# Kernel optimization log

Measured on AMD Instinct MI355X. Metric: run time of the kernel, lower is better.

## Reference

```python
import jax, jax.numpy as jnp
import numpy as np

B, S, L = 8, 64, 6          # graphs, spatial side, orientation layers
K = 6                       # Chebyshev order
IN_D, HID, OUT_D = 3, 128, 10


def _grid_edges(num_graphs, s, l):
    b, o, y, x = np.meshgrid(np.arange(num_graphs), np.arange(l), np.arange(s), np.arange(s), indexing='ij')
    nid = ((b * l + o) * s + y) * s + x  # linear node id, [B,L,s,s]
    srcs, dsts = [], []
    def add(a, c):
        srcs.append(a.ravel()); dsts.append(c.ravel())
    add(nid[..., :-1], nid[..., 1:]); add(nid[..., 1:], nid[..., :-1])                 # x-neighbors
    add(nid[:, :, :-1, :], nid[:, :, 1:, :]); add(nid[:, :, 1:, :], nid[:, :, :-1, :])  # y-neighbors
    nxt = np.roll(nid, -1, axis=1)                                                     # orientation ring
    add(nid, nxt); add(nxt, nid)
    return np.stack([np.concatenate(srcs), np.concatenate(dsts)]).astype(np.int32)


def _cluster_spatial(num_graphs, s, l):
    b, o, y, x = np.meshgrid(np.arange(num_graphs), np.arange(l), np.arange(s), np.arange(s), indexing='ij')
    h = s // 2
    return (((b * l + o) * h + y // 2) * h + x // 2).ravel().astype(np.int32)


def setup_inputs() -> dict:
    key = jax.random.key(0)
    ks = jax.random.split(key, 20)
    inp = {}
    N1 = B * L * S * S
    inp['x'] = jax.random.normal(ks[0], (N1, IN_D), jnp.float32)
    for i, s in enumerate([S, S // 2, S // 4]):
        ei = _grid_edges(B, s, L)
        inp[f'edge_index{i+1}'] = jnp.asarray(ei)
        inp[f'edge_attr{i+1}'] = jax.random.uniform(ks[1 + i], (ei.shape[1],), jnp.float32, 0.1, 1.0)
    inp['cluster1'] = jnp.asarray(_cluster_spatial(B, S, L))
    inp['cluster2'] = jnp.asarray(_cluster_spatial(B, S // 2, L))
    inp['cluster3'] = jnp.asarray(_cluster_spatial(B, S // 4, L))
    s4 = S // 8
    b, o, y, x = np.meshgrid(np.arange(B), np.arange(L), np.arange(s4), np.arange(s4), indexing='ij')
    inp['cluster4'] = jnp.asarray(((b * s4 + y) * s4 + x).ravel().astype(np.int32))  # collapse orientation axis
    inp['batch_final'] = jnp.asarray(np.repeat(np.arange(B), s4 * s4).astype(np.int32))
    dims = [(IN_D, HID), (HID, HID), (HID, HID), (HID, HID), (HID, HID), (HID, OUT_D)]
    for i, (di, do) in enumerate(dims):
        inp[f'W{i+1}'] = jax.random.normal(ks[8 + i], (K, di, do), jnp.float32) / np.float32(np.sqrt(di * K))
        inp[f'b{i+1}'] = jnp.zeros((do,), jnp.float32)
    for i in range(5):
        inp[f'gamma{i+1}'] = jnp.ones((HID,), jnp.float32)
        inp[f'beta{i+1}'] = jnp.zeros((HID,), jnp.float32)
    return inp


def _cheb_conv(x, ei, ea, W, b):
    # Chebyshev polynomial graph conv: out = sum_k T_k(L) x @ W_k + b,
    # with T0=x, T1=Lx, Tk = 2 L T_{k-1} - T_{k-2}; L applied via edge gather/scatter.
    src, dst = ei[0], ei[1]
    n = x.shape[0]
    def lap(v):
        return jax.ops.segment_sum(ea[:, None] * v[src], dst, num_segments=n)
    Tx0 = x
    out = Tx0 @ W[0]
    Tx1 = lap(x)
    out = out + Tx1 @ W[1]
    for k in range(2, W.shape[0]):
        Tx2 = 2.0 * lap(Tx1) - Tx0
        out = out + Tx2 @ W[k]
        Tx0, Tx1 = Tx1, Tx2
    return out + b


def _bn(x, g, bt):
    # BatchNorm1d in training mode (batch statistics, biased variance, eps=1e-5)
    mu = x.mean(0)
    var = x.var(0)
    return g * (x - mu) * jax.lax.rsqrt(var + 1e-5) + bt


def reference(x, edge_index1, edge_attr1, edge_index2, edge_attr2, edge_index3, edge_attr3, cluster1, cluster2, cluster3, cluster4, batch_final, W1, b1, W2, b2, W3, b3, W4, b4, W5, b5, W6, b6, gamma1, beta1, gamma2, beta2, gamma3, beta3, gamma4, beta4, gamma5, beta5):
    h = jax.nn.relu(_bn(_cheb_conv(x, edge_index1, edge_attr1, W1, b1), gamma1, beta1))
    h = jax.nn.relu(_bn(_cheb_conv(h, edge_index1, edge_attr1, W2, b2), gamma2, beta2))
    h = jax.ops.segment_max(h, cluster1, num_segments=B * L * (S // 2) ** 2)
    h = jax.nn.relu(_bn(_cheb_conv(h, edge_index2, edge_attr2, W3, b3), gamma3, beta3))
    h = jax.nn.relu(_bn(_cheb_conv(h, edge_index2, edge_attr2, W4, b4), gamma4, beta4))
    h = jax.ops.segment_max(h, cluster2, num_segments=B * L * (S // 4) ** 2)
    h = jax.nn.relu(_bn(_cheb_conv(h, edge_index3, edge_attr3, W5, b5), gamma5, beta5))
    h = jax.nn.relu(_cheb_conv(h, edge_index3, edge_attr3, W6, b6))
    h = jax.ops.segment_max(h, cluster3, num_segments=B * L * (S // 8) ** 2)   # spatial pool 3
    h = jax.ops.segment_max(h, cluster4, num_segments=B * (S // 8) ** 2)        # orientation pool
    g = jax.ops.segment_max(h, batch_final, num_segments=B)                     # global max pool
    return jax.nn.log_softmax(g, axis=1)
```

## Files before the change

### kernel.cpp

```cpp
#include <hip/hip_runtime.h>
#include <math.h>

#define L_OR 6
#define N_BL 48

typedef unsigned short u16;
typedef __attribute__((ext_vector_type(8))) short s8v;
typedef __attribute__((ext_vector_type(4))) float f4v;

#define N1 196608
#define N2 49152
#define N3 12288
#define LSTRIDE 114688

__device__ u16   g_cat[(size_t)N1 * 768 + 1024];
__device__ u16   g_O[(size_t)N1 * 128];
__device__ float g_Tt[5 * (size_t)N1 * 3];
__device__ u16   g_Bt[4 * LSTRIDE];
__device__ u16   g_W6t[16 * 768];
__device__ float g_wt1[(size_t)N1 * 8];
__device__ float g_wt2[(size_t)N2 * 8];
__device__ float g_wt3[(size_t)N3 * 8];
__device__ float g_O10[(size_t)N3 * 10];
__device__ float g_part[1536 * 256];
__device__ float g_part2[64 * 256];
__device__ float g_gsc[128];
__device__ float g_gso[128];
__device__ unsigned g_cnt;

__device__ __forceinline__ float b2f(u16 v) {
    return __uint_as_float(((unsigned)v) << 16);
}
__device__ __forceinline__ u16 f2b(float f) {
    unsigned u = __float_as_uint(f);
    return (u16)((u + 0x7FFFu + ((u >> 16) & 1u)) >> 16);
}

__global__ __launch_bounds__(256)
void eaprep_all(float* __restrict__ wt1, float* __restrict__ wt2,
                float* __restrict__ wt3, const float* __restrict__ ea1,
                const float* __restrict__ ea2, const float* __restrict__ ea3)
{
    int idx = blockIdx.x * 256 + threadIdx.x;
    int S, n; float* wtab; const float* ea;
    if (idx < N1)            { S = 64; wtab = wt1; ea = ea1; n = idx; }
    else if (idx < N1 + N2)  { S = 32; wtab = wt2; ea = ea2; n = idx - N1; }
    else if (idx < N1 + N2 + N3) { S = 16; wtab = wt3; ea = ea3; n = idx - N1 - N2; }
    else return;
    int x = n % S, y = (n / S) % S, g = n / (S * S);
    int o = g % L_OR, b = g / L_OR;
    const int szx = N_BL * S * (S - 1);
    const int basex = (g * S + y) * (S - 1);
    float wxm = (x > 0)     ? ea[basex + x - 1] : 0.f;
    float wxp = (x < S - 1) ? ea[szx + basex + x] : 0.f;
    float wym = (y > 0)     ? ea[2 * szx + (g * (S - 1) + y - 1) * S + x] : 0.f;
    float wyp = (y < S - 1) ? ea[3 * szx + (g * (S - 1) + y) * S + x] : 0.f;
    int op_ = (o == 0) ? L_OR - 1 : o - 1;
    int on_ = (o == L_OR - 1) ? 0 : o + 1;
    int sp = ((b * L_OR + op_) * S + y) * S + x;
    int sn = ((b * L_OR + on_) * S + y) * S + x;
    float wom = ea[4 * szx + sp];
    float wop = ea[4 * szx + N_BL * S * S + n];
    float* w = wtab + (size_t)n * 8;
    w[0] = wxm; w[1] = wxp; w[2] = wym; w[3] = wyp; w[4] = wom; w[5] = wop;
    ((int*)w)[6] = sp - n;
    ((int*)w)[7] = sn - n;
}

template<int S>
__global__ __launch_bounds__(256)
void lap128b(u16* __restrict__ cat, int outSlot, int inSlot, int tppSlot,
             const float* __restrict__ wtab, float alpha)
{
    const int NN = N_BL * S * S;
    int node = blockIdx.x * 16 + (threadIdx.x >> 4);
    int c8   = threadIdx.x & 15;

    float4 wa = *(const float4*)(wtab + (size_t)node * 8);
    float4 wb = *(const float4*)(wtab + (size_t)node * 8 + 4);
    int dsp = __float_as_int(wb.z);
    int dsn = __float_as_int(wb.w);
    int sxm = (node > 0)      ? node - 1 : 0;
    int sxp = (node < NN - 1) ? node + 1 : node;
    int sym = (node >= S)     ? node - S : node;
    int syp = (node < NN - S) ? node + S : node;

    const int chOff = inSlot * 128 + c8 * 8;
    float a[8] = {0.f, 0.f, 0.f, 0.f, 0.f, 0.f, 0.f, 0.f};
    auto gather = [&](int src, float w) {
        s8v v = *(const s8v*)(cat + (size_t)src * 768 + chOff);
#pragma unroll
        for (int j = 0; j < 8; ++j) a[j] += w * b2f((u16)v[j]);
    };
    gather(sxm, wa.x); gather(sxp, wa.y); gather(sym, wa.z); gather(syp, wa.w);
    gather(node + dsp, wb.x); gather(node + dsn, wb.y);

    float r[8];
#pragma unroll
    for (int j = 0; j < 8; ++j) r[j] = alpha * a[j];
    if (tppSlot >= 0) {
        s8v t = *(const s8v*)(cat + (size_t)node * 768 + tppSlot * 128 + c8 * 8);
#pragma unroll
        for (int j = 0; j < 8; ++j) r[j] -= b2f((u16)t[j]);
    }
    uint4 ov;
    asm("v_cvt_pk_bf16_f32 %0, %1, %2" : "=v"(ov.x) : "v"(r[0]), "v"(r[1]));
    asm("v_cvt_pk_bf16_f32 %0, %1, %2" : "=v"(ov.y) : "v"(r[2]), "v"(r[3]));
    asm("v_cvt_pk_bf16_f32 %0, %1, %2" : "=v"(ov.z) : "v"(r[4]), "v"(r[5]));
    asm("v_cvt_pk_bf16_f32 %0, %1, %2" : "=v"(ov.w) : "v"(r[6]), "v"(r[7]));
    *(uint4*)(cat + (size_t)node * 768 + outSlot * 128 + c8 * 8) = ov;
}

template<int S>
__global__ __launch_bounds__(256)
void lap1bn(u16* __restrict__ cat, const u16* __restrict__ O,
            int t0Slot, int t1Slot, const float* __restrict__ wtab,
            const float* __restrict__ gsc, const float* __restrict__ gso)
{
    const int NN = N_BL * S * S;
    int node = blockIdx.x * 16 + (threadIdx.x >> 4);
    int c8   = threadIdx.x & 15;

    float4 wa = *(const float4*)(wtab + (size_t)node * 8);
    float4 wb = *(const float4*)(wtab + (size_t)node * 8 + 4);
    int dsp = __float_as_int(wb.z);
    int dsn = __float_as_int(wb.w);
    int sxm = (node > 0)      ? node - 1 : 0;
    int sxp = (node < NN - 1) ? node + 1 : node;
    int sym = (node >= S)     ? node - S : node;
    int syp = (node < NN - S) ? node + S : node;

    float sc[8], so[8];
    {
        float4 s0 = *(const float4*)(gsc + c8 * 8);
        float4 s1 = *(const float4*)(gsc + c8 * 8 + 4);
        float4 o0 = *(const float4*)(gso + c8 * 8);
        float4 o1 = *(const float4*)(gso + c8 * 8 + 4);
        sc[0]=s0.x; sc[1]=s0.y; sc[2]=s0.z; sc[3]=s0.w;
        sc[4]=s1.x; sc[5]=s1.y; sc[6]=s1.z; sc[7]=s1.w;
        so[0]=o0.x; so[1]=o0.y; so[2]=o0.z; so[3]=o0.w;
        so[4]=o1.x; so[5]=o1.y; so[6]=o1.z; so[7]=o1.w;
    }

    float a[8] = {0.f, 0.f, 0.f, 0.f, 0.f, 0.f, 0.f, 0.f};
    auto gatherbn = [&](int src, float w) {
        s8v v = *(const s8v*)(O + (size_t)src * 128 + c8 * 8);
#pragma unroll
        for (int j = 0; j < 8; ++j)
            a[j] += w * fmaxf(b2f((u16)v[j]) * sc[j] + so[j], 0.f);
    };
    gatherbn(sxm, wa.x); gatherbn(sxp, wa.y); gatherbn(sym, wa.z); gatherbn(syp, wa.w);
    gatherbn(node + dsp, wb.x); gatherbn(node + dsn, wb.y);

    float t0[8];
    {
        s8v v = *(const s8v*)(O + (size_t)node * 128 + c8 * 8);
#pragma unroll
        for (int j = 0; j < 8; ++j)
            t0[j] = fmaxf(b2f((u16)v[j]) * sc[j] + so[j], 0.f);
    }
    uint4 o0v, o1v;
    asm("v_cvt_pk_bf16_f32 %0, %1, %2" : "=v"(o0v.x) : "v"(t0[0]), "v"(t0[1]));
    asm("v_cvt_pk_bf16_f32 %0, %1, %2" : "=v"(o0v.y) : "v"(t0[2]), "v"(t0[3]));
    asm("v_cvt_pk_bf16_f32 %0, %1, %2" : "=v"(o0v.z) : "v"(t0[4]), "v"(t0[5]));
    asm("v_cvt_pk_bf16_f32 %0, %1, %2" : "=v"(o0v.w) : "v"(t0[6]), "v"(t0[7]));
    asm("v_cvt_pk_bf16_f32 %0, %1, %2" : "=v"(o1v.x) : "v"(a[0]), "v"(a[1]));
    asm("v_cvt_pk_bf16_f32 %0, %1, %2" : "=v"(o1v.y) : "v"(a[2]), "v"(a[3]));
    asm("v_cvt_pk_bf16_f32 %0, %1, %2" : "=v"(o1v.z) : "v"(a[4]), "v"(a[5]));
    asm("v_cvt_pk_bf16_f32 %0, %1, %2" : "=v"(o1v.w) : "v"(a[6]), "v"(a[7]));
    *(uint4*)(cat + (size_t)node * 768 + t0Slot * 128 + c8 * 8) = o0v;
    *(uint4*)(cat + (size_t)node * 768 + t1Slot * 128 + c8 * 8) = o1v;
}

template<int S>
__global__ __launch_bounds__(256)
void lap3_kernel(float* __restrict__ out, const float* __restrict__ in,
                 const float* __restrict__ tpp, const float* __restrict__ wtab,
                 float alpha)
{
    const int NN = N_BL * S * S;
    int n = blockIdx.x * 256 + threadIdx.x;
    if (n >= NN) return;
    float4 wa = *(const float4*)(wtab + (size_t)n * 8);
    float4 wb = *(const float4*)(wtab + (size_t)n * 8 + 4);
    int dsp = __float_as_int(wb.z);
    int dsn = __float_as_int(wb.w);
    int sxm = (n > 0)      ? n - 1 : 0;
    int sxp = (n < NN - 1) ? n + 1 : n;
    int sym = (n >= S)     ? n - S : n;
    int syp = (n < NN - S) ? n + S : n;

    float a0 = 0.f, a1 = 0.f, a2 = 0.f;
    auto gather = [&](int src, float w) {
        a0 += w * in[src * 3 + 0];
        a1 += w * in[src * 3 + 1];
        a2 += w * in[src * 3 + 2];
    };
    gather(sxm, wa.x); gather(sxp, wa.y); gather(sym, wa.z); gather(syp, wa.w);
    gather(n + dsp, wb.x); gather(n + dsn, wb.y);

    float r0 = alpha * a0, r1 = alpha * a1, r2 = alpha * a2;
    if (tpp) { r0 -= tpp[n * 3 + 0]; r1 -= tpp[n * 3 + 1]; r2 -= tpp[n * 3 + 2]; }
    out[n * 3 + 0] = r0; out[n * 3 + 1] = r1; out[n * 3 + 2] = r2;
}

__global__ __launch_bounds__(256)
void gemm_mfma_cat(u16* __restrict__ O, const u16* __restrict__ A,
                   const u16* __restrict__ Bf, const float* __restrict__ bias,
                   float* __restrict__ partials)
{
    __shared__ u16 Bs[2][8192];
    const int tid  = threadIdx.x;
    const int wave = tid >> 6;
    const int lane = tid & 63;
    const int lrow = lane & 15;
    const int kg   = lane >> 4;
    const int r0   = blockIdx.x * 128 + wave * 32;

    const u16* A0 = A + (size_t)(r0 + lrow) * 768 + kg * 8;
    const u16* A1 = A0 + (size_t)16 * 768;

    f4v acc[2][8] = {};

    auto stage = [&](int q, int slot) {
        const char* src = (const char*)(Bf + q * 8192) + wave * 4096 + lane * 16;
        char* dstb = (char*)(&Bs[slot][0]) + wave * 4096;
#pragma unroll
        for (int i = 0; i < 4; ++i)
            __builtin_amdgcn_global_load_lds(
                (const __attribute__((address_space(1))) unsigned*)(src + i * 1024),
                (__attribute__((address_space(3))) unsigned*)(dstb + i * 1024),
                16, 0, 0);
    };

    stage(0, 0);
    s8v a00 = *(const s8v*)(A0);
    s8v a10 = *(const s8v*)(A1);
    s8v a01 = *(const s8v*)(A0 + 32);
    s8v a11 = *(const s8v*)(A1 + 32);
    __syncthreads();

#pragma unroll 1
    for (int p = 0; p < 12; ++p) {
        stage(p + 1, (p + 1) & 1);
        s8v na00 = *(const s8v*)(A0 + (p + 1) * 64);
        s8v na10 = *(const s8v*)(A1 + (p + 1) * 64);
        s8v na01 = *(const s8v*)(A0 + (p + 1) * 64 + 32);
        s8v na11 = *(const s8v*)(A1 + (p + 1) * 64 + 32);
        const u16* bsl = &Bs[p & 1][0];
#pragma unroll
        for (int ct = 0; ct < 8; ++ct) {
            s8v b = *(const s8v*)&bsl[(ct * 64 + lane) * 8];
            acc[0][ct] = __builtin_amdgcn_mfma_f32_16x16x32_bf16(a00, b, acc[0][ct], 0, 0, 0);
            acc[1][ct] = __builtin_amdgcn_mfma_f32_16x16x32_bf16(a10, b, acc[1][ct], 0, 0, 0);
        }
#pragma unroll
        for (int ct = 0; ct < 8; ++ct) {
            s8v b = *(const s8v*)&bsl[4096 + (ct * 64 + lane) * 8];
            acc[0][ct] = __builtin_amdgcn_mfma_f32_16x16x32_bf16(a01, b, acc[0][ct], 0, 0, 0);
            acc[1][ct] = __builtin_amdgcn_mfma_f32_16x16x32_bf16(a11, b, acc[1][ct], 0, 0, 0);
        }
        __syncthreads();
        a00 = na00; a10 = na10; a01 = na01; a11 = na11;
    }

    __shared__ float sred[4][2][8][16];
    float cs[8], cq[8];
#pragma unroll
    for (int ct = 0; ct < 8; ++ct) { cs[ct] = 0.f; cq[ct] = 0.f; }

#pragma unroll
    for (int s = 0; s < 2; ++s)
#pragma unroll
        for (int ct = 0; ct < 8; ++ct) {
            int col = ct * 16 + lrow;
            float bv = bias[col];
#pragma unroll
            for (int j = 0; j < 4; ++j) {
                int row = r0 + s * 16 + kg * 4 + j;
                float v = acc[s][ct][j] + bv;
                O[(size_t)row * 128 + col] = f2b(v);
                cs[ct] += v; cq[ct] += v * v;
            }
        }
#pragma unroll
    for (int ct = 0; ct < 8; ++ct) {
        cs[ct] += __shfl_xor(cs[ct], 16); cs[ct] += __shfl_xor(cs[ct], 32);
        cq[ct] += __shfl_xor(cq[ct], 16); cq[ct] += __shfl_xor(cq[ct], 32);
    }
    if (lane < 16) {
#pragma unroll
        for (int ct = 0; ct < 8; ++ct) {
            sred[wave][0][ct][lane] = cs[ct];
            sred[wave][1][ct][lane] = cq[ct];
        }
    }
    __syncthreads();
    if (threadIdx.x < 128) {
        int ct = threadIdx.x >> 4, lr = threadIdx.x & 15;
        float S = 0.f, Q = 0.f;
#pragma unroll
        for (int w = 0; w < 4; ++w) { S += sred[w][0][ct][lr]; Q += sred[w][1][ct][lr]; }
        partials[blockIdx.x * 256 + threadIdx.x]       = S;
        partials[blockIdx.x * 256 + 128 + threadIdx.x] = Q;
    }
}

__global__ __launch_bounds__(256)
void wprep_all(const float* __restrict__ W2, const float* __restrict__ W3,
               const float* __restrict__ W4, const float* __restrict__ W5,
               const float* __restrict__ W6, u16* __restrict__ Bf,
               u16* __restrict__ W6t)
{
    int l = blockIdx.y;
    int idx = blockIdx.x * 256 + threadIdx.x;
    if (l == 4) {
        if (idx >= 16 * 768) return;
        int c = idx / 768, kk = idx % 768;
        int slot = kk >> 7, d = kk & 127;
        W6t[idx] = (c < 10) ? f2b(W6[(size_t)slot * 1280 + d * 10 + c]) : (u16)0;
        return;
    }
    const float* W = (l == 0) ? W2 : (l == 1) ? W3 : (l == 2) ? W4 : W5;
    int base = (l & 1) ? 5 : 0;
    int j    = idx & 7;
    int lane = (idx >> 3) & 63;
    int ct   = (idx >> 9) & 7;
    int k0s  = idx >> 12;
    int k    = k0s * 32 + (lane >> 4) * 8 + j;
    int col  = ct * 16 + (lane & 15);
    int slot = k >> 7, d = k & 127;
    int wk = slot - base; if (wk < 0) wk += 6;
    Bf[(size_t)l * LSTRIDE + idx] = f2b(W[(size_t)wk * 16384 + d * 128 + col]);
}

__global__ __launch_bounds__(256)
void l1gemm(u16* __restrict__ O, const float* __restrict__ T0,
            const float* __restrict__ Tt, const float* __restrict__ W,
            const float* __restrict__ bias, float* __restrict__ partials)
{
    __shared__ float Ts[128][18];
    __shared__ float sh[2][128], sh2[2][128];
    int tid = threadIdx.x;
    int rbase = blockIdx.x * 128;
    for (int i = tid; i < 128 * 18; i += 256) {
        int r = i / 18, t = i % 18;
        int k = t / 3, j = t % 3;
        Ts[r][t] = (k == 0) ? T0[(size_t)(rbase + r) * 3 + j]
                            : Tt[(size_t)(k - 1) * N1 * 3 + (size_t)(rbase + r) * 3 + j];
    }
    __syncthreads();
    int c = tid & 127, h = tid >> 7;
    float w[18];
#pragma unroll
    for (int k = 0; k < 6; ++k)
#pragma unroll
        for (int j = 0; j < 3; ++j) w[k * 3 + j] = W[(size_t)k * 384 + j * 128 + c];
    float bv = bias[c];
    float S = 0.f, Q = 0.f;
    for (int i = 0; i < 64; ++i) {
        int r = h * 64 + i;
        float acc = bv;
#pragma unroll
        for (int t = 0; t < 18; ++t) acc += Ts[r][t] * w[t];
        O[(size_t)(rbase + r) * 128 + c] = f2b(acc);
        S += acc; Q += acc * acc;
    }
    sh[h][c] = S; sh2[h][c] = Q;
    __syncthreads();
    if (tid < 128) {
        partials[blockIdx.x * 256 + tid]       = sh[0][tid] + sh[1][tid];
        partials[blockIdx.x * 256 + 128 + tid] = sh2[0][tid] + sh2[1][tid];
    }
}

__global__ __launch_bounds__(256)
void out10_cat(float* __restrict__ O10, const u16* __restrict__ cat,
               const u16* __restrict__ W6t, const float* __restrict__ bias)
{
    int col = threadIdx.x & 15;
    int row = blockIdx.x * 16 + (threadIdx.x >> 4);
    const u16* a = cat + (size_t)row * 768;
    const u16* w = W6t + (size_t)col * 768;
    float acc = 0.f;
#pragma unroll 4
    for (int k0 = 0; k0 < 768; k0 += 8) {
        s8v av = *(const s8v*)(a + k0);
        s8v wv = *(const s8v*)(w + k0);
#pragma unroll
        for (int j = 0; j < 8; ++j)
            acc += b2f((u16)av[j]) * b2f((u16)wv[j]);
    }
    if (col < 10)
        O10[(size_t)row * 10 + col] = fmaxf(acc + bias[col], 0.f);
}

__global__ __launch_bounds__(256)
void bn_reduce_f(const float* __restrict__ partials, int nblk, int N,
                 const float* __restrict__ g, const float* __restrict__ bt,
                 float* __restrict__ gsc, float* __restrict__ gso,
                 float* __restrict__ part2, unsigned* __restrict__ cnt)
{
    int tid = threadIdx.x;
    float S = 0.f;
#pragma unroll 4
    for (int b = blockIdx.x; b < nblk; b += 64)
        S += partials[(size_t)b * 256 + tid];
    part2[blockIdx.x * 256 + tid] = S;
    __threadfence();
    __syncthreads();
    __shared__ int last;
    if (tid == 0) last = (atomicAdd(cnt, 1u) == 63u) ? 1 : 0;
    __syncthreads();
    if (!last) return;
    __threadfence();
    int c = tid & 127, h = tid >> 7;
    float Sa = 0.f, Qa = 0.f;
#pragma unroll 8
    for (int b = h; b < 64; b += 2) {
        Sa += part2[b * 256 + c];
        Qa += part2[b * 256 + 128 + c];
    }
    __shared__ float shS[2][128], shQ[2][128];
    shS[h][c] = Sa; shQ[h][c] = Qa;
    __syncthreads();
    if (tid < 128) {
        float Sx = shS[0][tid] + shS[1][tid];
        float Qx = shQ[0][tid] + shQ[1][tid];
        float inv_n = 1.f / (float)N;
        float mu = Sx * inv_n;
        float var = Qx * inv_n - mu * mu;
        float is = rsqrtf(var + 1e-5f);
        float sc = is * g[tid];
        gsc[tid] = sc;
        gso[tid] = bt[tid] - mu * sc;
    }
    if (tid == 0) *cnt = 0u;
}

__global__ __launch_bounds__(256)
void bn_apply_pool8(const u16* __restrict__ O, u16* __restrict__ cat, int outSlot,
                    int s, int Nout,
                    const float* __restrict__ gsc, const float* __restrict__ gso)
{
    int idx = blockIdx.x * 256 + threadIdx.x;
    if (idx >= Nout * 16) return;
    int c8 = idx & 15;
    int n2 = idx >> 4;
    int h  = s >> 1;
    int x2 = n2 % h;
    int y2 = (n2 / h) % h;
    int gg = n2 / (h * h);
    int base = (gg * s + 2 * y2) * s + 2 * x2;
    s8v v0 = *(const s8v*)(O + (size_t)base * 128 + c8 * 8);
    s8v v1 = *(const s8v*)(O + (size_t)(base + 1) * 128 + c8 * 8);
    s8v v2 = *(const s8v*)(O + (size_t)(base + s) * 128 + c8 * 8);
    s8v v3 = *(const s8v*)(O + (size_t)(base + s + 1) * 128 + c8 * 8);
    s8v ov;
#pragma unroll
    for (int j = 0; j < 8; ++j) {
        int c = c8 * 8 + j;
        float sc = gsc[c], so = gso[c];
        float m =          b2f((u16)v0[j]) * sc + so;
        m = fmaxf(m, b2f((u16)v1[j]) * sc + so);
        m = fmaxf(m, b2f((u16)v2[j]) * sc + so);
        m = fmaxf(m, b2f((u16)v3[j]) * sc + so);
        ov[j] = (short)f2b(fmaxf(m, 0.f));
    }
    *(s8v*)(cat + (size_t)n2 * 768 + outSlot * 128 + c8 * 8) = ov;
}

__global__ __launch_bounds__(512)
void tail_fused(const float* __restrict__ O10, float* __restrict__ out)
{
    __shared__ float p4[512][10];
    __shared__ float G[8][10];
    __shared__ float rowm[8], rowl[8];
    int t = threadIdx.x;
    for (int i = t; i < 5120; i += 512) {
        int c = i % 10, n = i / 10;
        int x = n & 7, y = (n >> 3) & 7, b = n >> 6;
        float m = -INFINITY;
        for (int o = 0; o < L_OR; ++o) {
            int base = ((b * L_OR + o) * 16 + 2 * y) * 16 + 2 * x;
            m = fmaxf(m, O10[(size_t)base * 10 + c]);
            m = fmaxf(m, O10[(size_t)(base + 1) * 10 + c]);
            m = fmaxf(m, O10[(size_t)(base + 16) * 10 + c]);
            m = fmaxf(m, O10[(size_t)(base + 17) * 10 + c]);
        }
        p4[n][c] = m;
    }
    __syncthreads();
    if (t < 80) {
        int b = t / 10, c = t % 10;
        float m = -INFINITY;
        for (int p = 0; p < 64; ++p) m = fmaxf(m, p4[b * 64 + p][c]);
        G[b][c] = m;
    }
    __syncthreads();
    if (t < 8) {
        float m = -INFINITY;
        for (int c = 0; c < 10; ++c) m = fmaxf(m, G[t][c]);
        float s = 0.f;
        for (int c = 0; c < 10; ++c) s += expf(G[t][c] - m);
        rowm[t] = m; rowl[t] = logf(s);
    }
    __syncthreads();
    if (t < 80) {
        int b = t / 10, c = t % 10;
        out[t] = G[b][c] - rowm[b] - rowl[b];
    }
}

static void launch_lapb(u16* cat, int os, int is, int ts, const float* wtab,
                        int S, int N, float alpha, hipStream_t st)
{
    dim3 grid(N / 16), block(256);
    if (S == 64)      hipLaunchKernelGGL(lap128b<64>, grid, block, 0, st, cat, os, is, ts, wtab, alpha);
    else if (S == 32) hipLaunchKernelGGL(lap128b<32>, grid, block, 0, st, cat, os, is, ts, wtab, alpha);
    else              hipLaunchKernelGGL(lap128b<16>, grid, block, 0, st, cat, os, is, ts, wtab, alpha);
}

static void cheb_laps_b5(u16* cat, const float* wtab, int S, int N, hipStream_t st)
{
    for (int k = 1; k < 6; ++k) {
        int os = (k + 5) % 6;
        int is = (k - 1 + 5) % 6;
        int ts = (k >= 2) ? (k - 2 + 5) % 6 : -1;
        launch_lapb(cat, os, is, ts, wtab, S, N, (k == 1) ? 1.f : 2.f, st);
    }
}

static void cheb_laps_2to5(u16* cat, const float* wtab, int S, int N, hipStream_t st)
{
    for (int k = 2; k < 6; ++k)
        launch_lapb(cat, k, k - 1, k - 2, wtab, S, N, 2.f, st);
}

static void launch_lap1bn(u16* cat, const u16* O, const float* wtab,
                          const float* gsc, const float* gso,
                          int S, int N, hipStream_t st)
{
    dim3 grid(N / 16), block(256);
    if (S == 64)      hipLaunchKernelGGL(lap1bn<64>, grid, block, 0, st, cat, O, 0, 1, wtab, gsc, gso);
    else if (S == 32) hipLaunchKernelGGL(lap1bn<32>, grid, block, 0, st, cat, O, 0, 1, wtab, gsc, gso);
    else              hipLaunchKernelGGL(lap1bn<16>, grid, block, 0, st, cat, O, 0, 1, wtab, gsc, gso);
}

extern "C" void kernel_launch(void* const* d_in, const int* in_sizes, int n_in,
                              void* d_out, int out_size, void* d_ws, size_t ws_size,
                              hipStream_t stream)
{
    const float* x   = (const float*)d_in[0];
    const float* ea1 = (const float*)d_in[2];
    const float* ea2 = (const float*)d_in[4];
    const float* ea3 = (const float*)d_in[6];
    const float* W1  = (const float*)d_in[12];
    const float* b1  = (const float*)d_in[13];
    const float* W2  = (const float*)d_in[14];
    const float* b2  = (const float*)d_in[15];
    const float* W3  = (const float*)d_in[16];
    const float* b3  = (const float*)d_in[17];
    const float* W4  = (const float*)d_in[18];
    const float* b4  = (const float*)d_in[19];
    const float* W5  = (const float*)d_in[20];
    const float* b5  = (const float*)d_in[21];
    const float* W6  = (const float*)d_in[22];
    const float* b6  = (const float*)d_in[23];
    const float* g1  = (const float*)d_in[24];
    const float* be1 = (const float*)d_in[25];
    const float* g2  = (const float*)d_in[26];
    const float* be2 = (const float*)d_in[27];
    const float* g3  = (const float*)d_in[28];
    const float* be3 = (const float*)d_in[29];
    const float* g4  = (const float*)d_in[30];
    const float* be4 = (const float*)d_in[31];
    const float* g5  = (const float*)d_in[32];
    const float* be5 = (const float*)d_in[33];

    u16 *cat, *O, *Bt, *W6t;
    float *Tt, *O10, *part, *part2, *gsc, *gso, *wt1, *wt2, *wt3;
    unsigned* cnt;
    if (hipGetSymbolAddress((void**)&cat, HIP_SYMBOL(g_cat)) != hipSuccess) return;
    if (hipGetSymbolAddress((void**)&O,   HIP_SYMBOL(g_O))   != hipSuccess) return;
    if (hipGetSymbolAddress((void**)&Tt,  HIP_SYMBOL(g_Tt))  != hipSuccess) return;
    if (hipGetSymbolAddress((void**)&Bt,  HIP_SYMBOL(g_Bt))  != hipSuccess) return;
    if (hipGetSymbolAddress((void**)&W6t, HIP_SYMBOL(g_W6t)) != hipSuccess) return;
    if (hipGetSymbolAddress((void**)&O10, HIP_SYMBOL(g_O10)) != hipSuccess) return;
    if (hipGetSymbolAddress((void**)&part,  HIP_SYMBOL(g_part))  != hipSuccess) return;
    if (hipGetSymbolAddress((void**)&part2, HIP_SYMBOL(g_part2)) != hipSuccess) return;
    if (hipGetSymbolAddress((void**)&gsc, HIP_SYMBOL(g_gsc)) != hipSuccess) return;
    if (hipGetSymbolAddress((void**)&gso, HIP_SYMBOL(g_gso)) != hipSuccess) return;
    if (hipGetSymbolAddress((void**)&wt1, HIP_SYMBOL(g_wt1)) != hipSuccess) return;
    if (hipGetSymbolAddress((void**)&wt2, HIP_SYMBOL(g_wt2)) != hipSuccess) return;
    if (hipGetSymbolAddress((void**)&wt3, HIP_SYMBOL(g_wt3)) != hipSuccess) return;
    if (hipGetSymbolAddress((void**)&cnt, HIP_SYMBOL(g_cnt)) != hipSuccess) return;

    dim3 blk(256);

    hipLaunchKernelGGL(eaprep_all, dim3((N1 + N2 + N3) / 256), blk, 0, stream,
                       wt1, wt2, wt3, ea1, ea2, ea3);
    hipLaunchKernelGGL(wprep_all, dim3(384, 5), blk, 0, stream, W2, W3, W4, W5, W6, Bt, W6t);

    {
        float* t1 = Tt;
        float* t2 = Tt + (size_t)N1 * 3;
        float* t3 = Tt + (size_t)2 * N1 * 3;
        float* t4 = Tt + (size_t)3 * N1 * 3;
        float* t5 = Tt + (size_t)4 * N1 * 3;
        dim3 gl((N1 + 255) / 256);
        hipLaunchKernelGGL(lap3_kernel<64>, gl, blk, 0, stream, t1, x,  (const float*)nullptr, wt1, 1.f);
        hipLaunchKernelGGL(lap3_kernel<64>, gl, blk, 0, stream, t2, t1, x,  wt1, 2.f);
        hipLaunchKernelGGL(lap3_kernel<64>, gl, blk, 0, stream, t3, t2, t1, wt1, 2.f);
        hipLaunchKernelGGL(lap3_kernel<64>, gl, blk, 0, stream, t4, t3, t2, wt1, 2.f);
        hipLaunchKernelGGL(lap3_kernel<64>, gl, blk, 0, stream, t5, t4, t3, wt1, 2.f);
        hipLaunchKernelGGL(l1gemm, dim3(N1 / 128), blk, 0, stream, O, x, Tt, W1, b1, part);
    }
    hipLaunchKernelGGL(bn_reduce_f, dim3(64), blk, 0, stream, part, N1 / 128, N1,
                       g1, be1, gsc, gso, part2, cnt);

    launch_lap1bn(cat, O, wt1, gsc, gso, 64, N1, stream);
    cheb_laps_2to5(cat, wt1, 64, N1, stream);
    hipLaunchKernelGGL(gemm_mfma_cat, dim3(N1 / 128), blk, 0, stream, O, cat, Bt, b2, part);
    hipLaunchKernelGGL(bn_reduce_f, dim3(64), blk, 0, stream, part, N1 / 128, N1,
                       g2, be2, gsc, gso, part2, cnt);
    hipLaunchKernelGGL(bn_apply_pool8, dim3(N2 / 16), blk, 0, stream,
                       O, cat, 5, 64, N2, gsc, gso);

    cheb_laps_b5(cat, wt2, 32, N2, stream);
    hipLaunchKernelGGL(gemm_mfma_cat, dim3(N2 / 128), blk, 0, stream, O, cat, Bt + 1 * LSTRIDE, b3, part);
    hipLaunchKernelGGL(bn_reduce_f, dim3(64), blk, 0, stream, part, N2 / 128, N2,
                       g3, be3, gsc, gso, part2, cnt);

    launch_lap1bn(cat, O, wt2, gsc, gso, 32, N2, stream);
    cheb_laps_2to5(cat, wt2, 32, N2, stream);
    hipLaunchKernelGGL(gemm_mfma_cat, dim3(N2 / 128), blk, 0, stream, O, cat, Bt + 2 * LSTRIDE, b4, part);
    hipLaunchKernelGGL(bn_reduce_f, dim3(64), blk, 0, stream, part, N2 / 128, N2,
                       g4, be4, gsc, gso, part2, cnt);
    hipLaunchKernelGGL(bn_apply_pool8, dim3(N3 / 16), blk, 0, stream,
                       O, cat, 5, 32, N3, gsc, gso);

    cheb_laps_b5(cat, wt3, 16, N3, stream);
    hipLaunchKernelGGL(gemm_mfma_cat, dim3(N3 / 128), blk, 0, stream, O, cat, Bt + 3 * LSTRIDE, b5, part);
    hipLaunchKernelGGL(bn_reduce_f, dim3(64), blk, 0, stream, part, N3 / 128, N3,
                       g5, be5, gsc, gso, part2, cnt);

    launch_lap1bn(cat, O, wt3, gsc, gso, 16, N3, stream);
    cheb_laps_2to5(cat, wt3, 16, N3, stream);
    hipLaunchKernelGGL(out10_cat, dim3(N3 / 16), blk, 0, stream, O10, cat, W6t, b6);

    hipLaunchKernelGGL(tail_fused, dim3(1), dim3(512), 0, stream, O10, (float*)d_out);
}
```

Before: 795.1 us.

## Swizzle Laplacian block order and stage GEMM B tiles through registers

The Laplacian kernels remap each block index so that consecutive blocks fall into eight strided node ranges. This is meant to change the order in which nodes are visited and how their neighbor gathers hit L2. The GEMM drops the direct global-to-LDS async loads. It now prefetches the next B tile into registers, then writes it to the other LDS buffer behind an extra barrier. That adds a second __syncthreads per iteration and more register pressure in exchange for ordinary vector loads.

After: 736.4 us (median of 2 runs). -7.4%, faster.

```diff
diff --git a/kernel.cpp b/kernel.cpp
--- a/kernel.cpp
+++ b/kernel.cpp
@@ -72,8 +72,11 @@
 void lap128b(u16* __restrict__ cat, int outSlot, int inSlot, int tppSlot,
              const float* __restrict__ wtab, float alpha)
 {
-    const int NN = N_BL * S * S;
-    int node = blockIdx.x * 16 + (threadIdx.x >> 4);
+    const int NN  = N_BL * S * S;
+    const int NWG = NN / 16;
+    int bid = blockIdx.x;
+    int sb  = (bid & 7) * (NWG >> 3) + (bid >> 3);
+    int node = sb * 16 + (threadIdx.x >> 4);
     int c8   = threadIdx.x & 15;
 
     float4 wa = *(const float4*)(wtab + (size_t)node * 8);
@@ -117,8 +120,11 @@
             int t0Slot, int t1Slot, const float* __restrict__ wtab,
             const float* __restrict__ gsc, const float* __restrict__ gso)
 {
-    const int NN = N_BL * S * S;
-    int node = blockIdx.x * 16 + (threadIdx.x >> 4);
+    const int NN  = N_BL * S * S;
+    const int NWG = NN / 16;
+    int bid = blockIdx.x;
+    int sb  = (bid & 7) * (NWG >> 3) + (bid >> 3);
+    int node = sb * 16 + (threadIdx.x >> 4);
     int c8   = threadIdx.x & 15;
 
     float4 wa = *(const float4*)(wtab + (size_t)node * 8);
@@ -222,18 +228,9 @@
 
     f4v acc[2][8] = {};
 
-    auto stage = [&](int q, int slot) {
-        const char* src = (const char*)(Bf + q * 8192) + wave * 4096 + lane * 16;
-        char* dstb = (char*)(&Bs[slot][0]) + wave * 4096;
-#pragma unroll
-        for (int i = 0; i < 4; ++i)
-            __builtin_amdgcn_global_load_lds(
-                (const __attribute__((address_space(1))) unsigned*)(src + i * 1024),
-                (__attribute__((address_space(3))) unsigned*)(dstb + i * 1024),
-                16, 0, 0);
-    };
-
-    stage(0, 0);
+#pragma unroll
+    for (int i = 0; i < 4; ++i)
+        *(s8v*)&Bs[0][i * 2048 + tid * 8] = *(const s8v*)(Bf + i * 2048 + tid * 8);
     s8v a00 = *(const s8v*)(A0);
     s8v a10 = *(const s8v*)(A1);
     s8v a01 = *(const s8v*)(A0 + 32);
@@ -242,24 +239,33 @@
 
 #pragma unroll 1
     for (int p = 0; p < 12; ++p) {
-        stage(p + 1, (p + 1) & 1);
+        const int cur = p & 1, nxt = cur ^ 1;
+        const u16* src = Bf + (p + 1) * 8192;
+        s8v nb0 = *(const s8v*)(src + tid * 8);
+        s8v nb1 = *(const s8v*)(src + 2048 + tid * 8);
+        s8v nb2 = *(const s8v*)(src + 4096 + tid * 8);
+        s8v nb3 = *(const s8v*)(src + 6144 + tid * 8);
         s8v na00 = *(const s8v*)(A0 + (p + 1) * 64);
         s8v na10 = *(const s8v*)(A1 + (p + 1) * 64);
         s8v na01 = *(const s8v*)(A0 + (p + 1) * 64 + 32);
         s8v na11 = *(const s8v*)(A1 + (p + 1) * 64 + 32);
-        const u16* bsl = &Bs[p & 1][0];
 #pragma unroll
         for (int ct = 0; ct < 8; ++ct) {
-            s8v b = *(const s8v*)&bsl[(ct * 64 + lane) * 8];
+            s8v b = *(const s8v*)&Bs[cur][(ct * 64 + lane) * 8];
             acc[0][ct] = __builtin_amdgcn_mfma_f32_16x16x32_bf16(a00, b, acc[0][ct], 0, 0, 0);
             acc[1][ct] = __builtin_amdgcn_mfma_f32_16x16x32_bf16(a10, b, acc[1][ct], 0, 0, 0);
         }
 #pragma unroll
         for (int ct = 0; ct < 8; ++ct) {
-            s8v b = *(const s8v*)&bsl[4096 + (ct * 64 + lane) * 8];
+            s8v b = *(const s8v*)&Bs[cur][4096 + (ct * 64 + lane) * 8];
             acc[0][ct] = __builtin_amdgcn_mfma_f32_16x16x32_bf16(a01, b, acc[0][ct], 0, 0, 0);
             acc[1][ct] = __builtin_amdgcn_mfma_f32_16x16x32_bf16(a11, b, acc[1][ct], 0, 0, 0);
         }
+        __syncthreads();
+        *(s8v*)&Bs[nxt][tid * 8]        = nb0;
+        *(s8v*)&Bs[nxt][2048 + tid * 8] = nb1;
+        *(s8v*)&Bs[nxt][4096 + tid * 8] = nb2;
+        *(s8v*)&Bs[nxt][6144 + tid * 8] = nb3;
         __syncthreads();
         a00 = na00; a10 = na10; a01 = na01; a11 = na11;
     }
```
